# Performance work log

Measured on AMD Instinct MI355X. Metric: run time of the kernel, lower is better.

Reference implementation:

```python
import jax, jax.numpy as jnp
import numpy as np


def setup_inputs() -> dict:
    key = jax.random.key(0)
    k1, k2 = jax.random.split(key)
    p1 = jax.random.normal(k1, (4, 8192, 3), dtype=jnp.float32)
    p2 = jax.random.normal(k2, (4, 8192, 3), dtype=jnp.float32)
    return {"p1": p1, "p2": p2}


def reference(p1, p2):
    # dist[b, n, m] = ||p1[b, n] - p2[b, m]||^2  (faithful to broadcasted diff)
    diff = p1[:, :, None, :] - p2[:, None, :, :]          # [B, N, M, 3]
    dist = jnp.sum(diff * diff, axis=-1)                  # [B, N, M]
    p1_to_p2 = jnp.min(dist, axis=-1)                     # [B, N]
    p2_to_p1 = jnp.min(dist, axis=-2)                     # [B, M]
    chamfer = (p1_to_p2.mean(axis=-1) + p2_to_p1.mean(axis=-1)).mean()
    return chamfer
```

## Files before the change

### kernel.cpp

```cpp
#include <hip/hip_runtime.h>

#define THREADS 256
#define QPT 4
#define Q2  (QPT / 2)
#define SLICES 16
#define NPTS 8192
#define BATCH 4
#define SLICE (NPTS / SLICES)

typedef float f2 __attribute__((ext_vector_type(2)));


__global__ void chamfer_init(unsigned int* mins, float* out) {
    int i = blockIdx.x * blockDim.x + threadIdx.x;
    mins[i] = 0x7F800000u;
    if (i == 0) out[0] = 0.0f;
}

__global__ __launch_bounds__(THREADS) void chamfer_main(
    const float* __restrict__ p1, const float* __restrict__ p2,
    unsigned int* __restrict__ mins)
{
    const int tid  = threadIdx.x;
    const int bz   = blockIdx.z;
    const int dir  = bz >> 2;
    const int b    = bz & 3;
    const int qbase = blockIdx.x * (THREADS * QPT);
    const int tbase = blockIdx.y * SLICE;

    const float* __restrict__ qsrc = (dir == 0) ? p1 : p2;
    const float* __restrict__ tsrc = (dir == 0) ? p2 : p1;

    __shared__ float4 tgt[SLICE];
    {
        const float* tp = tsrc + ((size_t)b * NPTS + tbase) * 3;
        for (int k = tid; k < SLICE; k += THREADS) {
            float x = tp[k * 3 + 0];
            float y = tp[k * 3 + 1];
            float z = tp[k * 3 + 2];
            tgt[k] = make_float4(-2.0f * x, -2.0f * y, -2.0f * z,
                                 fmaf(x, x, fmaf(y, y, z * z)));
        }
    }

    f2 ax2[Q2], ay2[Q2], az2[Q2], a2q[Q2], best2[Q2];
#pragma unroll
    for (int j = 0; j < Q2; ++j) {
        const int qa = qbase + (2 * j + 0) * THREADS + tid;
        const int qb = qbase + (2 * j + 1) * THREADS + tid;
        const float* pa = qsrc + ((size_t)b * NPTS + qa) * 3;
        const float* pb = qsrc + ((size_t)b * NPTS + qb) * 3;
        ax2[j] = f2{pa[0], pb[0]};
        ay2[j] = f2{pa[1], pb[1]};
        az2[j] = f2{pa[2], pb[2]};
        a2q[j].x = fmaf(ax2[j].x, ax2[j].x, fmaf(ay2[j].x, ay2[j].x, az2[j].x * az2[j].x));
        a2q[j].y = fmaf(ax2[j].y, ax2[j].y, fmaf(ay2[j].y, ay2[j].y, az2[j].y * az2[j].y));
        best2[j] = f2{3.0e38f, 3.0e38f};
    }

    __syncthreads();

#pragma unroll 4
    for (int m = 0; m < SLICE; m += 2) {
        float4 ta = tgt[m];
        float4 tb = tgt[m + 1];
        f2 tax = {ta.x, ta.x}, tay = {ta.y, ta.y}, taz = {ta.z, ta.z}, taw = {ta.w, ta.w};
        f2 tbx = {tb.x, tb.x}, tby = {tb.y, tb.y}, tbz = {tb.z, tb.z}, tbw = {tb.w, tb.w};
#pragma unroll
        for (int j = 0; j < Q2; ++j) {
            f2 da = __builtin_elementwise_fma(ax2[j], tax,
                     __builtin_elementwise_fma(ay2[j], tay,
                      __builtin_elementwise_fma(az2[j], taz, taw)));
            f2 db = __builtin_elementwise_fma(ax2[j], tbx,
                     __builtin_elementwise_fma(ay2[j], tby,
                      __builtin_elementwise_fma(az2[j], tbz, tbw)));
            best2[j].x = fminf(fminf(best2[j].x, da.x), db.x);
            best2[j].y = fminf(fminf(best2[j].y, da.y), db.y);
        }
    }

    unsigned int* mbase = mins + ((size_t)dir * BATCH + b) * NPTS;
#pragma unroll
    for (int j = 0; j < Q2; ++j) {
        float va = fmaxf(best2[j].x + a2q[j].x, 0.0f);
        float vb = fmaxf(best2[j].y + a2q[j].y, 0.0f);
        atomicMin(&mbase[qbase + (2 * j + 0) * THREADS + tid], __float_as_uint(va));
        atomicMin(&mbase[qbase + (2 * j + 1) * THREADS + tid], __float_as_uint(vb));
    }
}

__global__ __launch_bounds__(THREADS) void chamfer_reduce(
    const uint4* __restrict__ mins, float* __restrict__ out)
{
    const int i = blockIdx.x * THREADS + threadIdx.x;
    uint4 u = mins[i];
    float s = __uint_as_float(u.x) + __uint_as_float(u.y)
            + __uint_as_float(u.z) + __uint_as_float(u.w);
#pragma unroll
    for (int off = 32; off >= 1; off >>= 1)
        s += __shfl_down(s, off, 64);
    __shared__ float partial[THREADS / 64];
    if ((threadIdx.x & 63) == 0) partial[threadIdx.x >> 6] = s;
    __syncthreads();
    if (threadIdx.x == 0) {
        float tot = 0.0f;
#pragma unroll
        for (int w = 0; w < THREADS / 64; ++w) tot += partial[w];
        atomicAdd(out, tot * (1.0f / (BATCH * NPTS)));
    }
}

extern "C" void kernel_launch(void* const* d_in, const int* in_sizes, int n_in,
                              void* d_out, int out_size, void* d_ws, size_t ws_size,
                              hipStream_t stream) {
    const float* p1 = (const float*)d_in[0];
    const float* p2 = (const float*)d_in[1];
    unsigned int* mins = (unsigned int*)d_ws;
    float* out = (float*)d_out;

    chamfer_init<<<(2 * BATCH * NPTS) / THREADS, THREADS, 0, stream>>>(mins, out);

    dim3 grid(NPTS / (THREADS * QPT), SLICES, 2 * BATCH);
    chamfer_main<<<grid, THREADS, 0, stream>>>(p1, p2, mins);

    chamfer_reduce<<<(2 * BATCH * NPTS) / (4 * THREADS), THREADS, 0, stream>>>(
        (const uint4*)mins, out);
}
```

Measured before the change: 98.89 us.

## Fuse init, distance and reduce kernels with last-block reduction; retile queries

Replaces the three-kernel pipeline with one kernel. A memset initializes the workspace, including a block counter. The last block to finish, found through an atomic counter and threadfences, sums all per-point minima. Each thread now handles 16 queries instead of 4 over 64 smaller target slices, which raises register reuse of each shared-memory target load. The aim is to remove the extra launches and improve arithmetic intensity, at the cost of a serialized single-block final reduction done through 65536 atomic reads and higher register pressure.

```diff
diff --git a/kernel.cpp b/kernel.cpp
--- a/kernel.cpp
+++ b/kernel.cpp
@@ -1,30 +1,29 @@
 #include <hip/hip_runtime.h>
 
 #define THREADS 256
-#define QPT 4
-#define Q2  (QPT / 2)
-#define SLICES 16
+#define QPT 16
+#define QP2 (QPT / 2)
+#define SLICES 64
 #define NPTS 8192
 #define BATCH 4
 #define SLICE (NPTS / SLICES)
+#define NMINS (2 * BATCH * NPTS)
+#define NBLOCKS ((NPTS / (THREADS * QPT)) * SLICES * 2 * BATCH)
 
 typedef float f2 __attribute__((ext_vector_type(2)));
 
 
-__global__ void chamfer_init(unsigned int* mins, float* out) {
-    int i = blockIdx.x * blockDim.x + threadIdx.x;
-    mins[i] = 0x7F800000u;
-    if (i == 0) out[0] = 0.0f;
-}
+__global__ __launch_bounds__(THREADS, 4) void chamfer_fused(
+    const float* __restrict__ p1, const float* __restrict__ p2,
+    unsigned int* __restrict__ wsu, float* __restrict__ out)
+{
+    unsigned int* ctr  = wsu;
+    unsigned int* mins = wsu + 64;
 
-__global__ __launch_bounds__(THREADS) void chamfer_main(
-    const float* __restrict__ p1, const float* __restrict__ p2,
-    unsigned int* __restrict__ mins)
-{
     const int tid  = threadIdx.x;
-    const int bz   = blockIdx.z;
-    const int dir  = bz >> 2;
-    const int b    = bz & 3;
+    const int dirb = blockIdx.z;
+    const int dir  = dirb >> 2;
+    const int b    = dirb & 3;
     const int qbase = blockIdx.x * (THREADS * QPT);
     const int tbase = blockIdx.y * SLICE;
 
@@ -43,9 +42,9 @@
         }
     }
 
-    f2 ax2[Q2], ay2[Q2], az2[Q2], a2q[Q2], best2[Q2];
+    f2 ax2[QP2], ay2[QP2], az2[QP2], best2[QP2];
 #pragma unroll
-    for (int j = 0; j < Q2; ++j) {
+    for (int j = 0; j < QP2; ++j) {
         const int qa = qbase + (2 * j + 0) * THREADS + tid;
         const int qb = qbase + (2 * j + 1) * THREADS + tid;
         const float* pa = qsrc + ((size_t)b * NPTS + qa) * 3;
@@ -53,21 +52,19 @@
         ax2[j] = f2{pa[0], pb[0]};
         ay2[j] = f2{pa[1], pb[1]};
         az2[j] = f2{pa[2], pb[2]};
-        a2q[j].x = fmaf(ax2[j].x, ax2[j].x, fmaf(ay2[j].x, ay2[j].x, az2[j].x * az2[j].x));
-        a2q[j].y = fmaf(ax2[j].y, ax2[j].y, fmaf(ay2[j].y, ay2[j].y, az2[j].y * az2[j].y));
         best2[j] = f2{3.0e38f, 3.0e38f};
     }
 
     __syncthreads();
 
-#pragma unroll 4
+#pragma unroll 2
     for (int m = 0; m < SLICE; m += 2) {
         float4 ta = tgt[m];
         float4 tb = tgt[m + 1];
         f2 tax = {ta.x, ta.x}, tay = {ta.y, ta.y}, taz = {ta.z, ta.z}, taw = {ta.w, ta.w};
         f2 tbx = {tb.x, tb.x}, tby = {tb.y, tb.y}, tbz = {tb.z, tb.z}, tbw = {tb.w, tb.w};
 #pragma unroll
-        for (int j = 0; j < Q2; ++j) {
+        for (int j = 0; j < QP2; ++j) {
             f2 da = __builtin_elementwise_fma(ax2[j], tax,
                      __builtin_elementwise_fma(ay2[j], tay,
                       __builtin_elementwise_fma(az2[j], taz, taw)));
@@ -79,34 +76,53 @@
         }
     }
 
-    unsigned int* mbase = mins + ((size_t)dir * BATCH + b) * NPTS;
+    unsigned int* mbase = mins + ((size_t)dirb * NPTS);
 #pragma unroll
-    for (int j = 0; j < Q2; ++j) {
-        float va = fmaxf(best2[j].x + a2q[j].x, 0.0f);
-        float vb = fmaxf(best2[j].y + a2q[j].y, 0.0f);
+    for (int j = 0; j < QP2; ++j) {
+        f2 a2;
+        a2.x = fmaf(ax2[j].x, ax2[j].x, fmaf(ay2[j].x, ay2[j].x, az2[j].x * az2[j].x));
+        a2.y = fmaf(ax2[j].y, ax2[j].y, fmaf(ay2[j].y, ay2[j].y, az2[j].y * az2[j].y));
+        float va = fmaxf(best2[j].x + a2.x, 0.0f);
+        float vb = fmaxf(best2[j].y + a2.y, 0.0f);
         atomicMin(&mbase[qbase + (2 * j + 0) * THREADS + tid], __float_as_uint(va));
         atomicMin(&mbase[qbase + (2 * j + 1) * THREADS + tid], __float_as_uint(vb));
     }
-}
 
-__global__ __launch_bounds__(THREADS) void chamfer_reduce(
-    const uint4* __restrict__ mins, float* __restrict__ out)
-{
-    const int i = blockIdx.x * THREADS + threadIdx.x;
-    uint4 u = mins[i];
-    float s = __uint_as_float(u.x) + __uint_as_float(u.y)
-            + __uint_as_float(u.z) + __uint_as_float(u.w);
+    __threadfence();
+    __syncthreads();
+    __shared__ int is_last;
+    if (tid == 0) {
+        unsigned int old = atomicAdd(ctr, 1u);
+        is_last = (old == (unsigned int)(NBLOCKS - 2));
+    }
+    __syncthreads();
+    if (!is_last) return;
+    __threadfence();
+
+    float s0 = 0.f, s1 = 0.f, s2 = 0.f, s3 = 0.f;
+#pragma unroll 4
+    for (int k = 0; k < NMINS / THREADS; k += 4) {
+        unsigned int v0 = atomicMin(&mins[(k + 0) * THREADS + tid], 0xFFFFFFFFu);
+        unsigned int v1 = atomicMin(&mins[(k + 1) * THREADS + tid], 0xFFFFFFFFu);
+        unsigned int v2 = atomicMin(&mins[(k + 2) * THREADS + tid], 0xFFFFFFFFu);
+        unsigned int v3 = atomicMin(&mins[(k + 3) * THREADS + tid], 0xFFFFFFFFu);
+        s0 += __uint_as_float(v0);
+        s1 += __uint_as_float(v1);
+        s2 += __uint_as_float(v2);
+        s3 += __uint_as_float(v3);
+    }
+    float s = (s0 + s1) + (s2 + s3);
 #pragma unroll
     for (int off = 32; off >= 1; off >>= 1)
         s += __shfl_down(s, off, 64);
     __shared__ float partial[THREADS / 64];
-    if ((threadIdx.x & 63) == 0) partial[threadIdx.x >> 6] = s;
+    if ((tid & 63) == 0) partial[tid >> 6] = s;
     __syncthreads();
-    if (threadIdx.x == 0) {
+    if (tid == 0) {
         float tot = 0.0f;
 #pragma unroll
         for (int w = 0; w < THREADS / 64; ++w) tot += partial[w];
-        atomicAdd(out, tot * (1.0f / (BATCH * NPTS)));
+        out[0] = tot * (1.0f / (BATCH * NPTS));
     }
 }
 
@@ -115,14 +131,10 @@
                               hipStream_t stream) {
     const float* p1 = (const float*)d_in[0];
     const float* p2 = (const float*)d_in[1];
-    unsigned int* mins = (unsigned int*)d_ws;
     float* out = (float*)d_out;
 
-    chamfer_init<<<(2 * BATCH * NPTS) / THREADS, THREADS, 0, stream>>>(mins, out);
+    hipMemsetAsync(d_ws, 0xFF, 256 + (size_t)NMINS * 4, stream);
 
     dim3 grid(NPTS / (THREADS * QPT), SLICES, 2 * BATCH);
-    chamfer_main<<<grid, THREADS, 0, stream>>>(p1, p2, mins);
-
-    chamfer_reduce<<<(2 * BATCH * NPTS) / (4 * THREADS), THREADS, 0, stream>>>(
-        (const uint4*)mins, out);
+    chamfer_fused<<<grid, THREADS, 0, stream>>>(p1, p2, (unsigned int*)d_ws, out);
 }
```

Measured after the change: 171.7 us. 1.74x slower.
